# Kernel tuning notes

Hardware: AMD Instinct MI355X
Metric: run time of the kernel (lower is better)

Reference implementation:

```python
import jax, jax.numpy as jnp
import numpy as np

N = 100000   # nodes
E = 600000   # edges
H = 128      # hidden_size
G = 4000     # graphs in batch
T = 128      # num_tasks
ATOM_DIMS = np.array([119, 5, 12, 12, 10, 6, 6, 2, 2])  # OGB atom feature vocab sizes
OFFSETS = jnp.asarray(np.concatenate([[0], np.cumsum(ATOM_DIMS)[:-1]]), dtype=jnp.int64)


def setup_inputs() -> dict:
    key = jax.random.key(0)
    ks = jax.random.split(key, 12)
    x = jax.random.randint(ks[0], (N, 9), 0, 2)
    edge_index = jax.random.randint(ks[1], (2, E), 0, N)
    batch = jnp.sort(jax.random.randint(ks[2], (N,), 0, G))
    s = 1.0 / np.sqrt(H)
    atom_emb = jax.random.normal(ks[3], (int(ATOM_DIMS.sum()), H), dtype=jnp.float32) * 0.02
    W1 = jax.random.normal(ks[4], (H, H), dtype=jnp.float32) * s
    b1 = jnp.zeros((H,), dtype=jnp.float32)
    W2 = jax.random.normal(ks[5], (H, H), dtype=jnp.float32) * s
    b2 = jnp.zeros((H,), dtype=jnp.float32)
    W3 = jax.random.normal(ks[6], (H, H), dtype=jnp.float32) * s
    b3 = jnp.zeros((H,), dtype=jnp.float32)
    Wl = jax.random.normal(ks[7], (H, T), dtype=jnp.float32) * s
    bl = jnp.zeros((T,), dtype=jnp.float32)
    return dict(x=x, edge_index=edge_index, batch=batch, atom_emb=atom_emb,
                W1=W1, b1=b1, W2=W2, b2=b2, W3=W3, b3=b3, Wl=Wl, bl=bl)


def _gcn_conv(h, W, b, src, dst, dinv):
    # GCNConv: linear transform, then symmetric-normalized scatter-add with self-loops
    h = h @ W                                        # [N,H]
    norm = dinv[src] * dinv[dst]                     # [E]
    msg = h[src] * norm[:, None]                     # [E,H]
    agg = jax.ops.segment_sum(msg, dst, num_segments=N)
    # self-loop contribution: norm_ii = dinv_i^2, weight 1
    return agg + (dinv * dinv)[:, None] * h + b


def reference(x, edge_index, batch, atom_emb, W1, b1, W2, b2, W3, b3, Wl, bl):
    src, dst = edge_index[0], edge_index[1]
    # degree with self-loops (edge_weight = 1)
    deg = jax.ops.segment_sum(jnp.ones((E,), dtype=atom_emb.dtype), dst, num_segments=N) + 1.0
    dinv = jax.lax.rsqrt(deg)
    # AtomEncoder: sum of per-feature embeddings (one concatenated table + offsets)
    h = atom_emb[x + OFFSETS[None, :]].sum(axis=1)   # [N,H]
    h = jax.nn.relu(_gcn_conv(h, W1, b1, src, dst, dinv))
    h = jax.nn.relu(_gcn_conv(h, W2, b2, src, dst, dinv))
    h = _gcn_conv(h, W3, b3, src, dst, dinv)
    # global mean pool over graphs
    cnt = jax.ops.segment_sum(jnp.ones((N,), dtype=h.dtype), batch, num_segments=G)
    pooled = jax.ops.segment_sum(h, batch, num_segments=G) / jnp.maximum(cnt, 1.0)[:, None]
    return pooled @ Wl + bl                          # [G,T]
```

## Files before the change

kernel.cpp:

```cpp
#include <hip/hip_runtime.h>

#define NN 100000
#define EE 600000
#define HH 128
#define GG 4000
#define TT 128
#define PAD 64

typedef short short8 __attribute__((ext_vector_type(8)));
typedef unsigned short ushort8v __attribute__((ext_vector_type(8)));
typedef float floatx4 __attribute__((ext_vector_type(4)));

static __device__ __forceinline__ float bf2f(unsigned short u) {
  union { unsigned int i; float f; } v; v.i = ((unsigned int)u) << 16; return v.f;
}
static __device__ __forceinline__ unsigned short f2bf(float f) {
  union { float f; unsigned int i; } v; v.f = f;
  unsigned int r = (v.i + 0x7FFFu + ((v.i >> 16) & 1u)) >> 16;
  return (unsigned short)r;
}

#define DB ((EE / 4 + 255) / 256)
#define NB ((NN + 255) / 256)
#define AGG_GRID (NN / 16)
#define ENCB (NN / 16)
#define WTB 128
#define WCB 128

__global__ __launch_bounds__(256) void fill_enc_wt_k(const int* __restrict__ ei,
                                                     int* __restrict__ cnt,
                                                     int* __restrict__ csr_pad,
                                                     const int* __restrict__ x,
                                                     const float* __restrict__ emb,
                                                     unsigned short* __restrict__ h0,
                                                     const float* __restrict__ W1,
                                                     const float* __restrict__ W2,
                                                     unsigned short* __restrict__ Wt,
                                                     const float* __restrict__ W3,
                                                     const float* __restrict__ Wl,
                                                     const float* __restrict__ b3,
                                                     const float* __restrict__ bl,
                                                     float* __restrict__ Wc,
                                                     float* __restrict__ bc) {
  if (blockIdx.x < DB) {
    int e4 = (blockIdx.x * 256 + threadIdx.x) * 4;
    if (e4 >= EE) return;
    int4 s = *(const int4*)(ei + e4);
    int4 d = *(const int4*)(ei + EE + e4);
    int o0 = atomicAdd(&cnt[d.x], 1);
    int o1 = atomicAdd(&cnt[d.y], 1);
    int o2 = atomicAdd(&cnt[d.z], 1);
    int o3 = atomicAdd(&cnt[d.w], 1);
    if (o0 < PAD) csr_pad[d.x * PAD + o0] = s.x;
    if (o1 < PAD) csr_pad[d.y * PAD + o1] = s.y;
    if (o2 < PAD) csr_pad[d.z * PAD + o2] = s.z;
    if (o3 < PAD) csr_pad[d.w * PAD + o3] = s.w;
  } else if (blockIdx.x < DB + ENCB) {
    const int lane = threadIdx.x & 63;
    const int wid  = threadIdx.x >> 6;
    const int l16  = lane & 15;
    const int n = (blockIdx.x - DB) * 16 + wid * 4 + (lane >> 4);
    const int off[9] = {0, 119, 124, 136, 148, 158, 164, 170, 172};
    int xv = (l16 < 9) ? x[n * 9 + l16] : 0;
    float s[8] = {0.f, 0.f, 0.f, 0.f, 0.f, 0.f, 0.f, 0.f};
#pragma unroll
    for (int f = 0; f < 9; f++) {
      int idx = __shfl(xv, (lane & 48) | f, 64) + off[f];
      const float* ep = emb + (size_t)idx * HH + l16 * 8;
      float4 e0 = *(const float4*)ep;
      float4 e1 = *(const float4*)(ep + 4);
      s[0] += e0.x; s[1] += e0.y; s[2] += e0.z; s[3] += e0.w;
      s[4] += e1.x; s[5] += e1.y; s[6] += e1.z; s[7] += e1.w;
    }
    ushort8v o;
#pragma unroll
    for (int j = 0; j < 8; j++) o[j] = f2bf(s[j]);
    *(ushort8v*)(h0 + (size_t)n * HH + l16 * 8) = o;
  } else if (blockIdx.x < DB + ENCB + WTB) {
    int f = (blockIdx.x - DB - ENCB) * 256 + threadIdx.x;
    int wsel = f >> 14;
    int r = (f >> 7) & 127;
    int k = f & 127;
    const float* W = (wsel == 0) ? W1 : W2;
    Wt[wsel * HH * HH + r * HH + k] = f2bf(W[k * HH + r]);
  } else if (blockIdx.x < DB + ENCB + WTB + WCB) {
    const int h = blockIdx.x - DB - ENCB - WTB;
    const int t = threadIdx.x & 127;
    if (threadIdx.x >= 128) return;
    float acc = 0.f;
#pragma unroll 8
    for (int k = 0; k < HH; k++) acc += W3[h * HH + k] * Wl[k * TT + t];
    Wc[h * TT + t] = acc;
  } else {
    const int t = threadIdx.x & 127;
    if (threadIdx.x >= 128) return;
    float acc = bl[t];
#pragma unroll 8
    for (int k = 0; k < HH; k++) acc += b3[k] * Wl[k * TT + t];
    bc[t] = acc;
  }
}

template <bool L1GATHER>
__global__ __launch_bounds__(256) void agg_bf_k(const int* __restrict__ cnt,
                                                const int* __restrict__ csr_pad,
                                                const unsigned short* __restrict__ Hs,
                                                unsigned short* __restrict__ Aggs,
                                                const int* __restrict__ batch,
                                                int* __restrict__ gs) {
  if (L1GATHER && blockIdx.x >= AGG_GRID) {
    const int i = (blockIdx.x - AGG_GRID) * 256 + threadIdx.x;
    if (i < NN) {
      int b0 = batch[i];
      int b1 = (i + 1 < NN) ? batch[i + 1] : GG;
      for (int g = b0 + 1; g <= b1; g++) gs[g] = i + 1;
      if (i == 0)
        for (int g = 0; g <= b0; g++) gs[g] = 0;
    }
    return;
  }
  const int lane = threadIdx.x & 63;
  const int wid  = threadIdx.x >> 6;
  const int l16  = lane & 15;
  const int n = blockIdx.x * 16 + wid * 4 + (lane >> 4);
  const int deg = cnt[n];
  const int beg = n * PAD;
  const int end = beg + deg;
  const int last = end - 1;
  const float dn = rsqrtf((float)deg + 1.0f);
  float acc[8];
  {
    ushort8v v = *(const ushort8v*)(Hs + (size_t)n * HH + l16 * 8);
    const float sw = L1GATHER ? dn : 1.0f;
#pragma unroll
    for (int j = 0; j < 8; j++) acc[j] = sw * bf2f(v[j]);
  }
  int i = beg;
  if (i < end) {
    int c[8];
#pragma unroll
    for (int j = 0; j < 8; j++) c[j] = csr_pad[min(i + j, last)];
    while (true) {
      float m[8];
      m[0] = 1.f;
#pragma unroll
      for (int j = 1; j < 8; j++) m[j] = (i + j < end) ? 1.f : 0.f;
      if (L1GATHER) {
#pragma unroll
        for (int j = 0; j < 8; j++) m[j] *= rsqrtf((float)cnt[c[j]] + 1.0f);
      }
      ushort8v v[8];
#pragma unroll
      for (int j = 0; j < 8; j++)
        v[j] = *(const ushort8v*)(Hs + (size_t)c[j] * HH + l16 * 8);
      const int ni = i + 8;
      int p[8];
      if (ni < end) {
#pragma unroll
        for (int j = 0; j < 8; j++) p[j] = csr_pad[min(ni + j, last)];
      }
#pragma unroll
      for (int j = 0; j < 8; j++)
#pragma unroll
        for (int k = 0; k < 8; k++) acc[k] += m[j] * bf2f(v[j][k]);
      i = ni;
      if (i >= end) break;
#pragma unroll
      for (int j = 0; j < 8; j++) c[j] = p[j];
    }
  }
  ushort8v o;
#pragma unroll
  for (int j = 0; j < 8; j++) o[j] = f2bf(dn * acc[j]);
  *(ushort8v*)(Aggs + (size_t)n * HH + l16 * 8) = o;
}

__global__ __launch_bounds__(256) void gemm_mfma_k(const unsigned short* __restrict__ A,
                                                   const unsigned short* __restrict__ Wt,
                                                   const float* __restrict__ b,
                                                   const int* __restrict__ cnt,
                                                   unsigned short* __restrict__ Out) {
  const int w = threadIdx.x >> 6;
  const int l = threadIdx.x & 63;
  const int m16 = l & 15;
  const int q8  = (l >> 4) * 8;
  const int bm  = blockIdx.x * 128 + w * 32;

  floatx4 acc[2][8];
#pragma unroll
  for (int i = 0; i < 2; i++)
#pragma unroll
    for (int j = 0; j < 8; j++) acc[i][j] = (floatx4){0.f, 0.f, 0.f, 0.f};

  for (int q = 0; q < 4; q++) {
    const int k0 = q * 32;
    short8 a[2];
#pragma unroll
    for (int ti = 0; ti < 2; ti++) {
      int row = bm + ti * 16 + m16;
      a[ti] = (row < NN) ? *(const short8*)(A + (size_t)row * HH + k0 + q8)
                         : (short8){0, 0, 0, 0, 0, 0, 0, 0};
    }
#pragma unroll
    for (int tn = 0; tn < 8; tn++) {
      short8 bf = *(const short8*)(Wt + (size_t)(tn * 16 + m16) * HH + k0 + q8);
      acc[0][tn] = __builtin_amdgcn_mfma_f32_16x16x32_bf16(a[0], bf, acc[0][tn], 0, 0, 0);
      acc[1][tn] = __builtin_amdgcn_mfma_f32_16x16x32_bf16(a[1], bf, acc[1][tn], 0, 0, 0);
    }
  }

  float bias[8];
#pragma unroll
  for (int tn = 0; tn < 8; tn++) bias[tn] = b[tn * 16 + m16];

#pragma unroll
  for (int ti = 0; ti < 2; ti++) {
    const int rbase = bm + ti * 16 + (l >> 4) * 4;
#pragma unroll
    for (int r = 0; r < 4; r++) {
      const int row = rbase + r;
      if (row < NN) {
        const float dv = rsqrtf((float)cnt[row] + 1.0f);
#pragma unroll
        for (int tn = 0; tn < 8; tn++) {
          const int col = tn * 16 + m16;
          float v = acc[ti][tn][r] + bias[tn];
          v = dv * fmaxf(v, 0.f);
          Out[(size_t)row * HH + col] = f2bf(v);
        }
      }
    }
  }
}

__global__ __launch_bounds__(128) void pool_final_k(const int* __restrict__ gs,
                                                    const unsigned short* __restrict__ a3,
                                                    const float* __restrict__ Wc,
                                                    const float* __restrict__ bc,
                                                    float* __restrict__ out) {
  const int g = blockIdx.x;
  const int t = threadIdx.x;
  const int beg = gs[g];
  const int end = gs[g + 1];
  float s = 0.f;
  for (int n = beg; n < end; n++) s += bf2f(a3[(size_t)n * HH + t]);
  __shared__ float p[128];
  p[t] = s / (float)max(end - beg, 1);
  __syncthreads();
  float acc = bc[t];
#pragma unroll 8
  for (int h = 0; h < HH; h++) acc += p[h] * Wc[h * TT + t];
  out[(size_t)g * TT + t] = acc;
}

extern "C" void kernel_launch(void* const* d_in, const int* in_sizes, int n_in,
                              void* d_out, int out_size, void* d_ws, size_t ws_size,
                              hipStream_t stream) {
  const int*   x     = (const int*)d_in[0];
  const int*   ei    = (const int*)d_in[1];
  const int*   batch = (const int*)d_in[2];
  const float* emb   = (const float*)d_in[3];
  const float* W1    = (const float*)d_in[4];
  const float* b1    = (const float*)d_in[5];
  const float* W2    = (const float*)d_in[6];
  const float* b2    = (const float*)d_in[7];
  const float* W3    = (const float*)d_in[8];
  const float* b3    = (const float*)d_in[9];
  const float* Wl    = (const float*)d_in[10];
  const float* bl    = (const float*)d_in[11];
  float* out = (float*)d_out;

  unsigned short* bufA = (unsigned short*)d_ws;
  unsigned short* bufB = bufA + (size_t)NN * HH;
  unsigned short* Wt   = bufB + (size_t)NN * HH;
  float* Wc     = (float*)(Wt + 2 * HH * HH);
  float* bc     = Wc + HH * TT;
  int*   cnt    = (int*)(bc + TT);
  int*   gs     = cnt + NN;
  int*   csr    = gs + GG + 1;

  hipMemsetAsync(cnt, 0, NN * sizeof(int), stream);

  fill_enc_wt_k<<<DB + ENCB + WTB + WCB + 1, 256, 0, stream>>>(
      ei, cnt, csr, x, emb, bufA, W1, W2, Wt, W3, Wl, b3, bl, Wc, bc);

  const int gemm_grid = (NN + 127) / 128;

  agg_bf_k<true><<<AGG_GRID + NB, 256, 0, stream>>>(cnt, csr, bufA, bufB, batch, gs);
  gemm_mfma_k<<<gemm_grid, 256, 0, stream>>>(bufB, Wt, b1, cnt, bufA);

  agg_bf_k<false><<<AGG_GRID, 256, 0, stream>>>(cnt, csr, bufA, bufB, batch, gs);
  gemm_mfma_k<<<gemm_grid, 256, 0, stream>>>(bufB, Wt + HH * HH, b2, cnt, bufA);

  agg_bf_k<false><<<AGG_GRID, 256, 0, stream>>>(cnt, csr, bufA, bufB, batch, gs);

  pool_final_k<<<GG, 128, 0, stream>>>(gs, bufB, Wc, bc, out);
}
```

Baseline: 292.2 us.

## Fuse final aggregation layer with mean pooling and output projection

Replaces the last aggregation kernel and the separate pooling kernel with one kernel in which each wavefront handles a graph. It gathers neighbor rows for each node in the graph, scales them by the node's normalization, and accumulates directly into a pooled vector, so the aggregated layer-3 node features are never written out and read back. The W3·Wl precompute is also repacked to use all 256 threads across half as many blocks. The trade-off is parallelism: it now runs 1000 blocks with per-graph serial loops, where the old aggregation spread nodes across many more blocks, so load imbalance across graphs may hurt.

Measured after the change: 292.6 us. About the same (+0.1%).

```diff
diff --git a/kernel.cpp b/kernel.cpp
--- a/kernel.cpp
+++ b/kernel.cpp
@@ -9,6 +9,7 @@
 
 typedef short short8 __attribute__((ext_vector_type(8)));
 typedef unsigned short ushort8v __attribute__((ext_vector_type(8)));
+typedef unsigned short ushort4v __attribute__((ext_vector_type(4)));
 typedef float floatx4 __attribute__((ext_vector_type(4)));
 
 static __device__ __forceinline__ float bf2f(unsigned short u) {
@@ -25,7 +26,7 @@
 #define AGG_GRID (NN / 16)
 #define ENCB (NN / 16)
 #define WTB 128
-#define WCB 128
+#define WCB 64
 
 __global__ __launch_bounds__(256) void fill_enc_wt_k(const int* __restrict__ ei,
                                                      int* __restrict__ cnt,
@@ -84,9 +85,9 @@
     const float* W = (wsel == 0) ? W1 : W2;
     Wt[wsel * HH * HH + r * HH + k] = f2bf(W[k * HH + r]);
   } else if (blockIdx.x < DB + ENCB + WTB + WCB) {
-    const int h = blockIdx.x - DB - ENCB - WTB;
-    const int t = threadIdx.x & 127;
-    if (threadIdx.x >= 128) return;
+    int f = (blockIdx.x - DB - ENCB - WTB) * 256 + threadIdx.x;
+    const int h = f >> 7;
+    const int t = f & 127;
     float acc = 0.f;
 #pragma unroll 8
     for (int k = 0; k < HH; k++) acc += W3[h * HH + k] * Wl[k * TT + t];
@@ -233,24 +234,72 @@
   }
 }
 
-__global__ __launch_bounds__(128) void pool_final_k(const int* __restrict__ gs,
-                                                    const unsigned short* __restrict__ a3,
-                                                    const float* __restrict__ Wc,
-                                                    const float* __restrict__ bc,
-                                                    float* __restrict__ out) {
-  const int g = blockIdx.x;
-  const int t = threadIdx.x;
-  const int beg = gs[g];
-  const int end = gs[g + 1];
-  float s = 0.f;
-  for (int n = beg; n < end; n++) s += bf2f(a3[(size_t)n * HH + t]);
-  __shared__ float p[128];
-  p[t] = s / (float)max(end - beg, 1);
+__global__ __launch_bounds__(256) void agg_pool_k(const int* __restrict__ cnt,
+                                                  const int* __restrict__ csr_pad,
+                                                  const unsigned short* __restrict__ Hs,
+                                                  const int* __restrict__ gs,
+                                                  const float* __restrict__ Wc,
+                                                  const float* __restrict__ bc,
+                                                  float* __restrict__ out) {
+  __shared__ float p[4][HH];
+  const int w    = threadIdx.x >> 6;
+  const int lane = threadIdx.x & 63;
+  const int g    = blockIdx.x * 4 + w;
+  const int half = lane >> 5;
+  const int l32  = lane & 31;
+  const int beg = gs[g], endg = gs[g + 1];
+  float acc[4] = {0.f, 0.f, 0.f, 0.f};
+
+  for (int n = beg + half; n < endg; n += 2) {
+    const int deg = cnt[n];
+    const int eb = n * PAD;
+    const int ee = eb + deg;
+    const int el = ee - 1;
+    const float dn = rsqrtf((float)deg + 1.0f);
+    float rs[4];
+    {
+      ushort4v sv = *(const ushort4v*)(Hs + (size_t)n * HH + l32 * 4);
+#pragma unroll
+      for (int k = 0; k < 4; k++) rs[k] = bf2f(sv[k]);
+    }
+    for (int i = eb; i < ee; i += 8) {
+      int c[8]; float m[8];
+#pragma unroll
+      for (int j = 0; j < 8; j++) {
+        c[j] = csr_pad[min(i + j, el)];
+        m[j] = (i + j < ee) ? 1.f : 0.f;
+      }
+      ushort4v v[8];
+#pragma unroll
+      for (int j = 0; j < 8; j++)
+        v[j] = *(const ushort4v*)(Hs + (size_t)c[j] * HH + l32 * 4);
+#pragma unroll
+      for (int j = 0; j < 8; j++)
+#pragma unroll
+        for (int k = 0; k < 4; k++) rs[k] += m[j] * bf2f(v[j][k]);
+    }
+#pragma unroll
+    for (int k = 0; k < 4; k++) acc[k] += dn * rs[k];
+  }
+
+#pragma unroll
+  for (int k = 0; k < 4; k++) acc[k] += __shfl_xor(acc[k], 32, 64);
+  const float inv = 1.0f / (float)max(endg - beg, 1);
+  if (half == 0) {
+#pragma unroll
+    for (int k = 0; k < 4; k++) p[w][l32 * 4 + k] = acc[k] * inv;
+  }
   __syncthreads();
-  float acc = bc[t];
+
+  float a0 = bc[lane], a1 = bc[lane + 64];
 #pragma unroll 8
-  for (int h = 0; h < HH; h++) acc += p[h] * Wc[h * TT + t];
-  out[(size_t)g * TT + t] = acc;
+  for (int h = 0; h < HH; h++) {
+    const float ph = p[w][h];
+    a0 += ph * Wc[h * TT + lane];
+    a1 += ph * Wc[h * TT + lane + 64];
+  }
+  out[(size_t)g * TT + lane] = a0;
+  out[(size_t)g * TT + lane + 64] = a1;
 }
 
 extern "C" void kernel_launch(void* const* d_in, const int* in_sizes, int n_in,
@@ -292,7 +341,5 @@
   agg_bf_k<false><<<AGG_GRID, 256, 0, stream>>>(cnt, csr, bufA, bufB, batch, gs);
   gemm_mfma_k<<<gemm_grid, 256, 0, stream>>>(bufB, Wt + HH * HH, b2, cnt, bufA);
 
-  agg_bf_k<false><<<AGG_GRID, 256, 0, stream>>>(cnt, csr, bufA, bufB, batch, gs);
-
-  pool_final_k<<<GG, 128, 0, stream>>>(gs, bufB, Wc, bc, out);
-}
+  agg_pool_k<<<GG / 4, 256, 0, stream>>>(cnt, csr, bufA, gs, Wc, bc, out);
+}
```
